# Performance work log

Hardware: AMD Instinct MI355X
Metric: run time of the kernel (lower is better)

## Reference

```python
import jax, jax.numpy as jnp
import numpy as np

B, L, D, R = 8, 2048, 2048, 256
K = R if R % 2 == 1 else (R - 1 if R > 1 else 1)  # torch kernel-size rule -> 255


def setup_inputs() -> dict:
    key = jax.random.key(0)
    ks = jax.random.split(key, 6)
    x = jax.random.normal(ks[0], (B, L, D), dtype=jnp.float32)
    ln_gamma = jnp.ones((D,), jnp.float32)
    ln_beta = jnp.zeros((D,), jnp.float32)
    P_shared = jax.random.normal(ks[1], (D, R), jnp.float32) / np.float32(np.sqrt(D))
    dlt_T = jax.random.normal(ks[2], (R, R), jnp.float32) / np.float32(np.sqrt(R))
    phi_w = jax.random.normal(ks[3], (R,), jnp.float32)  # nn.Linear(1, r, bias=False) weight
    phi_bias = jnp.zeros((L, R), jnp.float32)            # created as zeros_like(phi_det)
    toep_params = jnp.ones((K,), jnp.float32) / np.float32(K)
    Wq = jax.random.normal(ks[4], (R, D), jnp.float32) / np.float32(np.sqrt(R))  # delta_Q: r->d
    bq = jnp.zeros((D,), jnp.float32)
    g_logit = jnp.array([-1.0, 0.0], jnp.float32)
    return {"x": x, "ln_gamma": ln_gamma, "ln_beta": ln_beta, "P_shared": P_shared,
            "dlt_T": dlt_T, "phi_w": phi_w, "phi_bias": phi_bias,
            "toep_params": toep_params, "Wq": Wq, "bq": bq, "g_logit": g_logit,
            "step": 5000}


def _layernorm(x, g, b, eps=1e-5):
    m = jnp.mean(x, -1, keepdims=True)
    v = jnp.mean((x - m) ** 2, -1, keepdims=True)
    return (x - m) * jax.lax.rsqrt(v + eps) * g + b


def _phi_det(Ll, Rr, dtype):
    # assumed phi_logic(t, L, r): DCT-II style deterministic phase table, shape (L, r)
    t = jnp.arange(Ll, dtype=dtype)[:, None]
    k = jnp.arange(Rr, dtype=dtype)[None, :]
    return jnp.cos(jnp.pi * (t + 0.5) * k / Ll)


def reference(x, ln_gamma, ln_beta, P_shared, dlt_T, phi_w, phi_bias,
              toep_params, Wq, bq, g_logit, step):
    Bb, Ll, Dd = x.shape
    Rr = P_shared.shape[1]
    x_norm = _layernorm(x, ln_gamma, ln_beta)
    phi_det = _phi_det(Ll, Rr, x.dtype)                      # (L, r)
    feat = jnp.mean(x_norm, -1, keepdims=True)               # (B, L, 1)
    phi_data = jnp.mean(feat * phi_w[None, None, :], axis=0)  # (L, r)
    det_scale = min(step / 2000.0, 1.0)                      # static Python scalar
    phi = det_scale * phi_det + phi_bias + phi_data          # (L, r)
    scale = jnp.sum(phi, axis=1) / jnp.float32(Rr)           # (L,)
    u = jnp.einsum('bld,dr->blr', x_norm, P_shared)          # SharedProj.forward_P
    z = jnp.einsum('blr,sr->bls', u, dlt_T)                  # DLT: fixed spectral transform
    # Toeplitz conv1d across spectral channels, padding 'same' (cross-correlation, as torch)
    zf = z.reshape(Bb * Ll, 1, Rr)
    mixed = jax.lax.conv_general_dilated(zf, toep_params[None, None, :], (1,), 'SAME',
                                         dimension_numbers=('NCH', 'OIH', 'NCH'))
    z_mixed = mixed.reshape(Bb, Ll, Rr)
    y = jnp.einsum('blr,rd->bld', z_mixed, Wq) + bq          # delta_Q
    g = jax.nn.sigmoid(g_logit)
    g = jnp.repeat(g, Dd // g.shape[0])                      # repeat_interleave to d_model
    # scale has L elements, broadcast over the FEATURE dim (L == d_model by construction)
    return g[None, None, :] * y * scale[None, None, :]
```

## Files before the change

### kernel.cpp

```cpp
#include <hip/hip_runtime.h>
#include <cstdint>
#include <math.h>

#define B_ 8
#define L_ 2048
#define D_ 2048
#define R_ 256

typedef __bf16 bf16x8 __attribute__((ext_vector_type(8)));
typedef float f32x4 __attribute__((ext_vector_type(4)));

__device__ __forceinline__ unsigned short f2bf(float f) {
    uint32_t u = __builtin_bit_cast(uint32_t, f);
    u += 0x7FFFu + ((u >> 16) & 1u);
    return (unsigned short)(u >> 16);
}

#define GLDS16(gp, lp)                                                          \
    __builtin_amdgcn_global_load_lds(                                           \
        (const __attribute__((address_space(1))) void*)(gp),                    \
        (__attribute__((address_space(3))) void*)(lp), 16, 0, 0)

__global__ __launch_bounds__(256) void ln_kernel(
    const float* __restrict__ x, const float* __restrict__ gamma,
    const float* __restrict__ beta, unsigned short* __restrict__ xn,
    float* __restrict__ feat)
{
    const int row  = blockIdx.x;
    const int t    = threadIdx.x;
    const int w    = t >> 6, lane = t & 63;
    const float4* x4 = (const float4*)(x + (size_t)row * D_);
    const float4* g4 = (const float4*)gamma;
    const float4* b4 = (const float4*)beta;
    float4 a  = x4[t];
    float4 b  = x4[t + 256];
    float4 g0 = g4[t], g1 = g4[t + 256];
    float4 e0 = b4[t], e1 = b4[t + 256];

    float s   = a.x + a.y + a.z + a.w + b.x + b.y + b.z + b.w;
    float sq  = a.x*a.x + a.y*a.y + a.z*a.z + a.w*a.w
              + b.x*b.x + b.y*b.y + b.z*b.z + b.w*b.w;
    float sxg = a.x*g0.x + a.y*g0.y + a.z*g0.z + a.w*g0.w
              + b.x*g1.x + b.y*g1.y + b.z*g1.z + b.w*g1.w;
    float sg  = g0.x + g0.y + g0.z + g0.w + g1.x + g1.y + g1.z + g1.w;
    float sb  = e0.x + e0.y + e0.z + e0.w + e1.x + e1.y + e1.z + e1.w;

    __shared__ float red[20];
#pragma unroll
    for (int o = 32; o; o >>= 1) {
        s   += __shfl_down(s, o);
        sq  += __shfl_down(sq, o);
        sxg += __shfl_down(sxg, o);
        sg  += __shfl_down(sg, o);
        sb  += __shfl_down(sb, o);
    }
    if (lane == 0) {
        red[w] = s; red[4+w] = sq; red[8+w] = sxg; red[12+w] = sg; red[16+w] = sb;
    }
    __syncthreads();
    float S    = red[0] + red[1] + red[2] + red[3];
    float SQ   = red[4] + red[5] + red[6] + red[7];
    float SXG  = red[8] + red[9] + red[10] + red[11];
    float SG   = red[12] + red[13] + red[14] + red[15];
    float SB   = red[16] + red[17] + red[18] + red[19];
    float mean = S * (1.0f / D_);
    float var  = SQ * (1.0f / D_) - mean * mean;
    float rstd = rsqrtf(var + 1e-5f);
    if (t == 0)
        feat[row] = (rstd * (SXG - mean * SG) + SB) * (1.0f / D_);

    float n[8];
    n[0] = (a.x - mean) * rstd * g0.x + e0.x;
    n[1] = (a.y - mean) * rstd * g0.y + e0.y;
    n[2] = (a.z - mean) * rstd * g0.z + e0.z;
    n[3] = (a.w - mean) * rstd * g0.w + e0.w;
    n[4] = (b.x - mean) * rstd * g1.x + e1.x;
    n[5] = (b.y - mean) * rstd * g1.y + e1.y;
    n[6] = (b.z - mean) * rstd * g1.z + e1.z;
    n[7] = (b.w - mean) * rstd * g1.w + e1.w;

    ushort4 o0, o1;
    o0.x = f2bf(n[0]); o0.y = f2bf(n[1]); o0.z = f2bf(n[2]); o0.w = f2bf(n[3]);
    o1.x = f2bf(n[4]); o1.y = f2bf(n[5]); o1.z = f2bf(n[6]); o1.w = f2bf(n[7]);
    ((ushort4*)(xn + (size_t)row * D_))[t]       = o0;
    ((ushort4*)(xn + (size_t)row * D_))[t + 256] = o1;
}

__global__ __launch_bounds__(256) void pt_kernel(
    const float* __restrict__ P, unsigned short* __restrict__ PT)
{
    __shared__ unsigned short sT[64 * 256];
    const int k0 = blockIdx.x * 64, t = threadIdx.x;
#pragma unroll 8
    for (int j = 0; j < 64; j++)
        sT[j * 256 + t] = f2bf(P[(size_t)(k0 + j) * R_ + t]);
    __syncthreads();
#pragma unroll
    for (int c = 0; c < 16; c++) {
        ushort4 v;
        v.x = sT[(c * 4 + 0) * 256 + t];
        v.y = sT[(c * 4 + 1) * 256 + t];
        v.z = sT[(c * 4 + 2) * 256 + t];
        v.w = sT[(c * 4 + 3) * 256 + t];
        *(ushort4*)(PT + (size_t)t * D_ + k0 + c * 4) = v;
    }
}

__global__ __launch_bounds__(256) void w2_kernel(
    const float* __restrict__ dlt, const float* __restrict__ toep,
    float* __restrict__ W2T)
{
    int s = blockIdx.x, q = threadIdx.x;
    int r0 = s - 127; if (r0 < 0) r0 = 0;
    int r1 = s + 127; if (r1 > 255) r1 = 255;
    float acc = 0.f;
    for (int r = r0; r <= r1; r++)
        acc += dlt[(size_t)r * R_ + q] * toep[r - s + 127];
    W2T[(size_t)s * R_ + q] = acc;
}

__global__ __launch_bounds__(256) void wt_kernel(
    const float* __restrict__ W2T, const float* __restrict__ Wq,
    unsigned short* __restrict__ WT)
{
    const int d0 = blockIdx.x * 4, q = threadIdx.x;
    float a0 = 0.f, a1 = 0.f, a2 = 0.f, a3 = 0.f;
    for (int s = 0; s < R_; s++) {
        float w2 = W2T[(size_t)s * R_ + q];
        const float* wr = Wq + (size_t)s * D_ + d0;
        a0 += w2 * wr[0]; a1 += w2 * wr[1]; a2 += w2 * wr[2]; a3 += w2 * wr[3];
    }
    WT[(size_t)(d0 + 0) * R_ + q] = f2bf(a0);
    WT[(size_t)(d0 + 1) * R_ + q] = f2bf(a1);
    WT[(size_t)(d0 + 2) * R_ + q] = f2bf(a2);
    WT[(size_t)(d0 + 3) * R_ + q] = f2bf(a3);
}

__global__ __launch_bounds__(256) void scale_kernel(
    const float* __restrict__ phi_bias, const float* __restrict__ phi_w,
    const float* __restrict__ feat, const float* __restrict__ bq,
    const float* __restrict__ g_logit, const int* __restrict__ step,
    float* __restrict__ gs, float* __restrict__ bgs)
{
    int l = blockIdx.x, k = threadIdx.x;
    int w = k >> 6, lane = k & 63;
    float arg = 3.14159265358979323846f * ((float)l + 0.5f) * (float)k * (1.0f / L_);
    float cv = cosf(arg);
    float pb = phi_bias[(size_t)l * R_ + k];
    float pw = phi_w[k];
    __shared__ float red[12];
#pragma unroll
    for (int o = 32; o; o >>= 1) {
        cv += __shfl_down(cv, o);
        pb += __shfl_down(pb, o);
        pw += __shfl_down(pw, o);
    }
    if (lane == 0) { red[w] = cv; red[4 + w] = pb; red[8 + w] = pw; }
    __syncthreads();
    if (k == 0) {
        float cs  = red[0] + red[1] + red[2] + red[3];
        float pbs = red[4] + red[5] + red[6] + red[7];
        float pws = red[8] + red[9] + red[10] + red[11];
        float fb = 0.f;
        for (int b = 0; b < B_; b++) fb += feat[(size_t)b * L_ + l];
        fb *= (1.0f / B_);
        float det = fminf((float)step[0] / 2000.0f, 1.0f);
        float sc  = (det * cs + pbs + fb * pws) * (1.0f / R_);
        float gl  = g_logit[l >> 10];
        float gg  = 1.0f / (1.0f + expf(-gl));
        gs[l]  = gg * sc;
        bgs[l] = bq[l] * gg * sc;
    }
}

__global__ __launch_bounds__(256, 2) void gemm1_kernel(
    const unsigned short* __restrict__ A,
    const unsigned short* __restrict__ BT,
    unsigned short* __restrict__ U)
{
    __shared__ __align__(16) unsigned short sA[2][64 * 32];
    __shared__ __align__(16) unsigned short sB[2][128 * 32];
    const int tid  = threadIdx.x;
    const int n0   = blockIdx.x * 128;
    const int m0   = blockIdx.y * 64;
    const int w    = tid >> 6, lane = tid & 63;
    const int quad = lane >> 4, m16 = lane & 15;
    const int wm   = (w >> 1) * 32, wn = (w & 1) * 64;
    const int ra   = tid >> 2, sa = tid & 3;

    f32x4 acc[2][4] = {};

    for (int kc = 0; kc < 2048; kc += 64) {
        const unsigned short* ap = A + (size_t)(m0 + ra) * 2048 + kc + sa * 8;
        GLDS16(ap,      sA[0] + tid * 8);
        GLDS16(ap + 32, sA[1] + tid * 8);
#pragma unroll
        for (int i = 0; i < 2; i++) {
            int idx = i * 256 + tid;
            int r = idx >> 2, seg = idx & 3;
            const unsigned short* bp = BT + (size_t)(n0 + r) * 2048 + kc + seg * 8;
            GLDS16(bp,      sB[0] + idx * 8);
            GLDS16(bp + 32, sB[1] + idx * 8);
        }
        __syncthreads();
#pragma unroll
        for (int h = 0; h < 2; h++) {
            bf16x8 af[2], bf[4];
#pragma unroll
            for (int i = 0; i < 2; i++)
                af[i] = *(const bf16x8*)(sA[h] + ((wm + i * 16 + m16) * 32 + quad * 8));
#pragma unroll
            for (int j = 0; j < 4; j++)
                bf[j] = *(const bf16x8*)(sB[h] + ((wn + j * 16 + m16) * 32 + quad * 8));
#pragma unroll
            for (int i = 0; i < 2; i++)
#pragma unroll
                for (int j = 0; j < 4; j++)
                    acc[i][j] = __builtin_amdgcn_mfma_f32_16x16x32_bf16(
                        af[i], bf[j], acc[i][j], 0, 0, 0);
        }
        __syncthreads();
    }

#pragma unroll
    for (int i = 0; i < 2; i++)
#pragma unroll
        for (int j = 0; j < 4; j++) {
            int col = n0 + wn + j * 16 + m16;
#pragma unroll
            for (int r = 0; r < 4; r++) {
                int row = m0 + wm + i * 16 + quad * 4 + r;
                U[(size_t)row * 256 + col] = f2bf(acc[i][j][r]);
            }
        }
}

__global__ __launch_bounds__(256, 3) void gemm2_kernel(
    const unsigned short* __restrict__ A,
    const unsigned short* __restrict__ BT,
    const float* __restrict__ gs, const float* __restrict__ bgs,
    float* __restrict__ out)
{
    __shared__ __align__(16) unsigned short sA[2][128 * 32];
    __shared__ __align__(16) unsigned short sB[2][128 * 32];
    const int tid  = threadIdx.x;
    const int n0   = blockIdx.x * 128;
    const int m0   = blockIdx.y * 128;
    const int w    = tid >> 6, lane = tid & 63;
    const int quad = lane >> 4, m16 = lane & 15;
    const int wm   = (w >> 1) * 64, wn = (w & 1) * 64;

    float gv[4], bv[4];
#pragma unroll
    for (int j = 0; j < 4; j++) {
        int col = n0 + wn + j * 16 + m16;
        gv[j] = gs[col];
        bv[j] = bgs[col];
    }

    f32x4 acc[4][4] = {};

    for (int kc = 0; kc < 256; kc += 64) {
#pragma unroll
        for (int i = 0; i < 2; i++) {
            int idx = i * 256 + tid;
            int r = idx >> 2, seg = idx & 3;
            const unsigned short* ap = A + (size_t)(m0 + r) * 256 + kc + seg * 8;
            const unsigned short* bp = BT + (size_t)(n0 + r) * 256 + kc + seg * 8;
            GLDS16(ap,      sA[0] + idx * 8);
            GLDS16(ap + 32, sA[1] + idx * 8);
            GLDS16(bp,      sB[0] + idx * 8);
            GLDS16(bp + 32, sB[1] + idx * 8);
        }
        __syncthreads();
#pragma unroll
        for (int h = 0; h < 2; h++) {
            bf16x8 af[4], bf[4];
#pragma unroll
            for (int i = 0; i < 4; i++)
                af[i] = *(const bf16x8*)(sA[h] + ((wm + i * 16 + m16) * 32 + quad * 8));
#pragma unroll
            for (int j = 0; j < 4; j++)
                bf[j] = *(const bf16x8*)(sB[h] + ((wn + j * 16 + m16) * 32 + quad * 8));
#pragma unroll
            for (int i = 0; i < 4; i++)
#pragma unroll
                for (int j = 0; j < 4; j++)
                    acc[i][j] = __builtin_amdgcn_mfma_f32_16x16x32_bf16(
                        af[i], bf[j], acc[i][j], 0, 0, 0);
        }
        __syncthreads();
    }

#pragma unroll
    for (int i = 0; i < 4; i++)
#pragma unroll
        for (int r = 0; r < 4; r++) {
            int row = m0 + wm + i * 16 + quad * 4 + r;
            float* op = out + (size_t)row * 2048 + n0 + wn;
#pragma unroll
            for (int j = 0; j < 4; j++)
                op[j * 16 + m16] = acc[i][j][r] * gv[j] + bv[j];
        }
}

extern "C" void kernel_launch(void* const* d_in, const int* in_sizes, int n_in,
                              void* d_out, int out_size, void* d_ws, size_t ws_size,
                              hipStream_t stream)
{
    const float* x        = (const float*)d_in[0];
    const float* ln_gamma = (const float*)d_in[1];
    const float* ln_beta  = (const float*)d_in[2];
    const float* P        = (const float*)d_in[3];
    const float* dlt      = (const float*)d_in[4];
    const float* phi_w    = (const float*)d_in[5];
    const float* phi_bias = (const float*)d_in[6];
    const float* toep     = (const float*)d_in[7];
    const float* Wq       = (const float*)d_in[8];
    const float* bq       = (const float*)d_in[9];
    const float* g_logit  = (const float*)d_in[10];
    const int*   step     = (const int*)d_in[11];
    float* out = (float*)d_out;

    char* w = (char*)d_ws;
    unsigned short* xn  = (unsigned short*)(w);
    unsigned short* u   = (unsigned short*)(w + 67108864);
    unsigned short* PT  = (unsigned short*)(w + 75497472);
    unsigned short* WT  = (unsigned short*)(w + 76546048);
    float*          W2T = (float*)(w + 77594624);
    float*          feat= (float*)(w + 77856768);
    float*          gs  = (float*)(w + 77922304);
    float*          bgs = (float*)(w + 77930496);

    ln_kernel<<<dim3(B_ * L_), dim3(256), 0, stream>>>(x, ln_gamma, ln_beta, xn, feat);
    pt_kernel<<<dim3(32), dim3(256), 0, stream>>>(P, PT);
    w2_kernel<<<dim3(R_), dim3(256), 0, stream>>>(dlt, toep, W2T);
    wt_kernel<<<dim3(512), dim3(256), 0, stream>>>(W2T, Wq, WT);
    scale_kernel<<<dim3(L_), dim3(256), 0, stream>>>(phi_bias, phi_w, feat, bq,
                                                     g_logit, step, gs, bgs);
    gemm1_kernel<<<dim3(2, 256), dim3(256), 0, stream>>>(xn, PT, u);
    gemm2_kernel<<<dim3(16, 128), dim3(256), 0, stream>>>(u, WT, gs, bgs, out);
}
```

Before: 392.0 us.

## Double-buffer LDS tiles in both GEMM kernels to overlap loads with MFMA

Both GEMM kernels now prefetch the next K-chunk into an alternate LDS buffer with async global-to-LDS loads while MFMAs run on the current buffer. This removes the per-iteration load-then-sync stall before compute. gemm1 keeps its 64-wide K step, so its LDS footprint doubles. gemm2 switches to a 32-wide K step with two buffers and keeps its LDS size. The price is more LDS in gemm1, which may cut occupancy, and more iterations and barriers in gemm2.

Result: slower. 400.6 us (+2.2%).

```diff
diff --git a/kernel.cpp b/kernel.cpp
--- a/kernel.cpp
+++ b/kernel.cpp
@@ -178,8 +178,8 @@
     const unsigned short* __restrict__ BT,
     unsigned short* __restrict__ U)
 {
-    __shared__ __align__(16) unsigned short sA[2][64 * 32];
-    __shared__ __align__(16) unsigned short sB[2][128 * 32];
+    __shared__ __align__(16) unsigned short sA[2][2][64 * 32];
+    __shared__ __align__(16) unsigned short sB[2][2][128 * 32];
     const int tid  = threadIdx.x;
     const int n0   = blockIdx.x * 128;
     const int m0   = blockIdx.y * 64;
@@ -188,30 +188,37 @@
     const int wm   = (w >> 1) * 32, wn = (w & 1) * 64;
     const int ra   = tid >> 2, sa = tid & 3;
 
+    const unsigned short* apb  = A  + (size_t)(m0 + ra) * 2048 + sa * 8;
+    const unsigned short* bpb0 = BT + (size_t)(n0 + ra) * 2048 + sa * 8;
+    const unsigned short* bpb1 = bpb0 + (size_t)64 * 2048;
+
     f32x4 acc[2][4] = {};
 
+#define G1_STAGE(buf, kc)                                              \
+    do {                                                               \
+        GLDS16(apb  + (kc),      &sA[buf][0][tid * 8]);                \
+        GLDS16(apb  + (kc) + 32, &sA[buf][1][tid * 8]);                \
+        GLDS16(bpb0 + (kc),      &sB[buf][0][tid * 8]);                \
+        GLDS16(bpb0 + (kc) + 32, &sB[buf][1][tid * 8]);                \
+        GLDS16(bpb1 + (kc),      &sB[buf][0][(256 + tid) * 8]);        \
+        GLDS16(bpb1 + (kc) + 32, &sB[buf][1][(256 + tid) * 8]);        \
+    } while (0)
+
+    G1_STAGE(0, 0);
+    __syncthreads();
+
+    int cur = 0;
     for (int kc = 0; kc < 2048; kc += 64) {
-        const unsigned short* ap = A + (size_t)(m0 + ra) * 2048 + kc + sa * 8;
-        GLDS16(ap,      sA[0] + tid * 8);
-        GLDS16(ap + 32, sA[1] + tid * 8);
-#pragma unroll
-        for (int i = 0; i < 2; i++) {
-            int idx = i * 256 + tid;
-            int r = idx >> 2, seg = idx & 3;
-            const unsigned short* bp = BT + (size_t)(n0 + r) * 2048 + kc + seg * 8;
-            GLDS16(bp,      sB[0] + idx * 8);
-            GLDS16(bp + 32, sB[1] + idx * 8);
-        }
-        __syncthreads();
+        if (kc + 64 < 2048) G1_STAGE(cur ^ 1, kc + 64);
 #pragma unroll
         for (int h = 0; h < 2; h++) {
             bf16x8 af[2], bf[4];
 #pragma unroll
             for (int i = 0; i < 2; i++)
-                af[i] = *(const bf16x8*)(sA[h] + ((wm + i * 16 + m16) * 32 + quad * 8));
+                af[i] = *(const bf16x8*)(&sA[cur][h][(wm + i * 16 + m16) * 32 + quad * 8]);
 #pragma unroll
             for (int j = 0; j < 4; j++)
-                bf[j] = *(const bf16x8*)(sB[h] + ((wn + j * 16 + m16) * 32 + quad * 8));
+                bf[j] = *(const bf16x8*)(&sB[cur][h][(wn + j * 16 + m16) * 32 + quad * 8]);
 #pragma unroll
             for (int i = 0; i < 2; i++)
 #pragma unroll
@@ -220,7 +227,9 @@
                         af[i], bf[j], acc[i][j], 0, 0, 0);
         }
         __syncthreads();
-    }
+        cur ^= 1;
+    }
+#undef G1_STAGE
 
 #pragma unroll
     for (int i = 0; i < 2; i++)
@@ -249,6 +258,12 @@
     const int w    = tid >> 6, lane = tid & 63;
     const int quad = lane >> 4, m16 = lane & 15;
     const int wm   = (w >> 1) * 64, wn = (w & 1) * 64;
+    const int ra   = tid >> 2, sa = tid & 3;
+
+    const unsigned short* apb0 = A  + (size_t)(m0 + ra) * 256 + sa * 8;
+    const unsigned short* apb1 = apb0 + (size_t)64 * 256;
+    const unsigned short* bpb0 = BT + (size_t)(n0 + ra) * 256 + sa * 8;
+    const unsigned short* bpb1 = bpb0 + (size_t)64 * 256;
 
     float gv[4], bv[4];
 #pragma unroll
@@ -260,37 +275,37 @@
 
     f32x4 acc[4][4] = {};
 
-    for (int kc = 0; kc < 256; kc += 64) {
-#pragma unroll
-        for (int i = 0; i < 2; i++) {
-            int idx = i * 256 + tid;
-            int r = idx >> 2, seg = idx & 3;
-            const unsigned short* ap = A + (size_t)(m0 + r) * 256 + kc + seg * 8;
-            const unsigned short* bp = BT + (size_t)(n0 + r) * 256 + kc + seg * 8;
-            GLDS16(ap,      sA[0] + idx * 8);
-            GLDS16(ap + 32, sA[1] + idx * 8);
-            GLDS16(bp,      sB[0] + idx * 8);
-            GLDS16(bp + 32, sB[1] + idx * 8);
-        }
+#define G2_STAGE(buf, kc)                                      \
+    do {                                                       \
+        GLDS16(apb0 + (kc), &sA[buf][tid * 8]);                \
+        GLDS16(apb1 + (kc), &sA[buf][(256 + tid) * 8]);        \
+        GLDS16(bpb0 + (kc), &sB[buf][tid * 8]);                \
+        GLDS16(bpb1 + (kc), &sB[buf][(256 + tid) * 8]);        \
+    } while (0)
+
+    G2_STAGE(0, 0);
+    __syncthreads();
+
+    int cur = 0;
+    for (int kc = 0; kc < 256; kc += 32) {
+        if (kc + 32 < 256) G2_STAGE(cur ^ 1, kc + 32);
+        bf16x8 af[4], bf[4];
+#pragma unroll
+        for (int i = 0; i < 4; i++)
+            af[i] = *(const bf16x8*)(&sA[cur][(wm + i * 16 + m16) * 32 + quad * 8]);
+#pragma unroll
+        for (int j = 0; j < 4; j++)
+            bf[j] = *(const bf16x8*)(&sB[cur][(wn + j * 16 + m16) * 32 + quad * 8]);
+#pragma unroll
+        for (int i = 0; i < 4; i++)
+#pragma unroll
+            for (int j = 0; j < 4; j++)
+                acc[i][j] = __builtin_amdgcn_mfma_f32_16x16x32_bf16(
+                    af[i], bf[j], acc[i][j], 0, 0, 0);
         __syncthreads();
-#pragma unroll
-        for (int h = 0; h < 2; h++) {
-            bf16x8 af[4], bf[4];
-#pragma unroll
-            for (int i = 0; i < 4; i++)
-                af[i] = *(const bf16x8*)(sA[h] + ((wm + i * 16 + m16) * 32 + quad * 8));
-#pragma unroll
-            for (int j = 0; j < 4; j++)
-                bf[j] = *(const bf16x8*)(sB[h] + ((wn + j * 16 + m16) * 32 + quad * 8));
-#pragma unroll
-            for (int i = 0; i < 4; i++)
-#pragma unroll
-                for (int j = 0; j < 4; j++)
-                    acc[i][j] = __builtin_amdgcn_mfma_f32_16x16x32_bf16(
-                        af[i], bf[j], acc[i][j], 0, 0, 0);
-        }
-        __syncthreads();
-    }
+        cur ^= 1;
+    }
+#undef G2_STAGE
 
 #pragma unroll
     for (int i = 0; i < 4; i++)
```
